# Kernel optimization log

Hardware: AMD Instinct MI355X
Metric: run time of the kernel (lower is better)

## Reference

```python
import jax, jax.numpy as jnp
import numpy as np

N = 6144
D_IN = 512
D_OUT = 512
DENSITY = 0.005


def setup_inputs() -> dict:
    key = jax.random.key(0)
    ks = jax.random.split(key, 12)
    x = jax.random.normal(ks[0], (N, D_IN), dtype=jnp.float32)
    adj_a = (jax.random.uniform(ks[1], (N, N)) < DENSITY).astype(jnp.float32)
    adj_b = (jax.random.uniform(ks[2], (N, N)) < DENSITY).astype(jnp.float32)
    # SparseAttention params (xavier-ish scale)
    W_sa = jax.random.normal(ks[3], (D_IN, D_OUT), dtype=jnp.float32) * (1.414 / np.sqrt(D_IN + D_OUT))
    a_sa = jax.random.normal(ks[4], (1, 2 * D_OUT), dtype=jnp.float32) * (1.414 / np.sqrt(1 + 2 * D_OUT))
    # GraphConvolution b params (uniform +-1/sqrt(out))
    stdv = 1.0 / np.sqrt(D_OUT)
    W_gcnb = jax.random.uniform(ks[5], (D_IN, D_OUT), minval=-stdv, maxval=stdv, dtype=jnp.float32)
    b_gcnb = jax.random.uniform(ks[6], (D_OUT,), minval=-stdv, maxval=stdv, dtype=jnp.float32)
    # gate Linear layers: Linear(2*D_IN, 1)
    s = 1.0 / np.sqrt(2 * D_IN)
    Wa = jax.random.uniform(ks[7], (1, 2 * D_IN), minval=-s, maxval=s, dtype=jnp.float32)
    ba = jax.random.uniform(ks[8], (1,), minval=-s, maxval=s, dtype=jnp.float32)
    Wb = jax.random.uniform(ks[9], (1, 2 * D_IN), minval=-s, maxval=s, dtype=jnp.float32)
    bb = jax.random.uniform(ks[10], (1,), minval=-s, maxval=s, dtype=jnp.float32)
    return {"x": x, "adj_a": adj_a, "adj_b": adj_b, "W_sa": W_sa, "a_sa": a_sa,
            "W_gcnb": W_gcnb, "b_gcnb": b_gcnb, "Wa": Wa, "ba": ba, "Wb": Wb, "bb": bb}


def reference(x, adj_a, adj_b, W_sa, a_sa, W_gcnb, b_gcnb, Wa, ba, Wb, bb):
    # type-level gates: sigmoid(Linear(cat[adj@x, x]))
    type_sum_a = adj_a @ x                      # [N, D_IN]
    type_sum_b = adj_b @ x
    attn_a = jax.nn.sigmoid(jnp.concatenate([type_sum_a, x], axis=1) @ Wa.T + ba)  # [N,1]
    attn_b = jax.nn.sigmoid(jnp.concatenate([type_sum_b, x], axis=1) @ Wb.T + bb)

    # SparseAttention over adj_a (edge pattern only)
    h = x @ W_sa                                # [N, D_OUT]
    Hd = h.shape[1]
    s_left = h @ a_sa[0, :Hd]                   # [N] contribution of source node i
    s_right = h @ a_sa[0, Hd:]                  # [N] contribution of target node j
    scores = s_left[:, None] + s_right[None, :]  # [N,N]
    e = jnp.where(adj_a != 0, jnp.exp(-jax.nn.leaky_relu(scores, 0.01)), 0.0)
    attn = e / (jnp.sum(e, axis=1, keepdims=True) + 1e-5)
    x_a = attn @ h                              # [N, D_OUT]

    # GCN branch over adj_b
    x_b = adj_b @ (x @ W_gcnb) + b_gcnb         # [N, D_OUT]

    return jax.nn.sigmoid(attn_a * x_a + attn_b * x_b)
```

## Files before the change

kernel.cpp:

```cpp
#include <hip/hip_runtime.h>
#include <math.h>

#define NN 6144
#define DD 512
#define CAP 128

typedef __bf16 bf16_t;
typedef __bf16 bf16x8 __attribute__((ext_vector_type(8)));
typedef unsigned short u16x8 __attribute__((ext_vector_type(8)));
typedef float f32x4 __attribute__((ext_vector_type(4)));

__device__ __forceinline__ float bf2f(unsigned short u) {
    unsigned v = ((unsigned)u) << 16;
    return __builtin_bit_cast(float, v);
}
__device__ __forceinline__ unsigned short f2bf(float f) {
    unsigned u = __builtin_bit_cast(unsigned, f);
    u += 0x7fffu + ((u >> 16) & 1u);
    return (unsigned short)(u >> 16);
}
__device__ __forceinline__ float sigmoidf_(float z) { return 1.0f / (1.0f + expf(-z)); }

__global__ __launch_bounds__(256) void k_prep(const float* __restrict__ Wsa,
                                              const float* __restrict__ Wg,
                                              const float* __restrict__ x,
                                              const float* __restrict__ Wa,
                                              const float* __restrict__ Wb,
                                              unsigned short* __restrict__ wt,
                                              float* __restrict__ xal, float* __restrict__ xar,
                                              float* __restrict__ xbl, float* __restrict__ xbr) {
    __shared__ float s[64][65];
    int bid = blockIdx.x;
    if (bid < 128) {
        int n0 = (bid & 15) * 64;
        int k0 = (bid >> 4) * 64;
        int tx = threadIdx.x & 63, ty = threadIdx.x >> 6;
        const float* src = (n0 < 512) ? Wsa : Wg;
        int nn0 = n0 & 511;
#pragma unroll
        for (int kk = 0; kk < 64; kk += 4)
            s[kk + ty][tx] = src[(size_t)(k0 + kk + ty) * 512 + nn0 + tx];
        __syncthreads();
#pragma unroll
        for (int nn = 0; nn < 64; nn += 4)
            wt[(size_t)(n0 + nn + ty) * 512 + k0 + tx] = f2bf(s[tx][nn + ty]);
    } else {
        int wave = threadIdx.x >> 6, lane = threadIdx.x & 63;
        int row = (bid - 128) * 4 + wave;
        int k0 = lane * 8;
        const float* xr_ = x + (size_t)row * DD + k0;
        float4 v0 = *(const float4*)xr_;
        float4 v1 = *(const float4*)(xr_ + 4);
        float xv[8] = {v0.x, v0.y, v0.z, v0.w, v1.x, v1.y, v1.z, v1.w};
        float a0 = 0, a1 = 0, b0 = 0, b1 = 0;
#pragma unroll
        for (int j = 0; j < 8; j++) {
            a0 += xv[j] * Wa[k0 + j];
            a1 += xv[j] * Wa[512 + k0 + j];
            b0 += xv[j] * Wb[k0 + j];
            b1 += xv[j] * Wb[512 + k0 + j];
        }
#pragma unroll
        for (int off = 32; off; off >>= 1) {
            a0 += __shfl_down(a0, off); a1 += __shfl_down(a1, off);
            b0 += __shfl_down(b0, off); b1 += __shfl_down(b1, off);
        }
        if (lane == 0) { xal[row] = a0; xar[row] = a1; xbl[row] = b0; xbr[row] = b1; }
    }
}

__global__ __launch_bounds__(256) void k_fused(const float* __restrict__ x,
                                               const bf16_t* __restrict__ wt,
                                               const float* __restrict__ adjA,
                                               const float* __restrict__ adjB,
                                               int* __restrict__ idxA, int* __restrict__ idxB,
                                               int* __restrict__ cntA, int* __restrict__ cntB,
                                               unsigned short* __restrict__ h,
                                               unsigned short* __restrict__ g) {
    int bid = blockIdx.x;
    int wave = threadIdx.x >> 6, lane = threadIdx.x & 63;
    int grp = bid % 5;
    if (grp < 4) {
        int sid = (bid / 5) * 4 + grp;
        int gw = sid * 4 + wave;
        int row = gw >> 1;
        int half = gw & 1;
        int which = row >= NN;
        int r = which ? row - NN : row;
        const float* adj = which ? adjB : adjA;
        int* idx = (which ? idxB : idxA) + (size_t)r * CAP;
        int* cnt = which ? cntB : cntA;

        const uint4* arow = (const uint4*)(adj + (size_t)r * NN) + half * 768 + lane;
        unsigned long long m = 0;
#pragma unroll
        for (int j = 0; j < 12; j++) {
            uint4 v = arow[j * 64];
            unsigned long long bits =
                (unsigned long long)(v.x != 0u) |
                ((unsigned long long)(v.y != 0u) << 1) |
                ((unsigned long long)(v.z != 0u) << 2) |
                ((unsigned long long)(v.w != 0u) << 3);
            m |= bits << (j * 4);
        }
        int c = (int)__popcll(m);
        int p = c;
#pragma unroll
        for (int off = 1; off < 64; off <<= 1) {
            int t = __shfl_up(p, off);
            if (lane >= off) p += t;
        }
        int total = __shfl(p, 63);
        int base = 0;
        if (lane == 0) base = atomicAdd(&cnt[r], total);
        base = __shfl(base, 0);
        int pos = base + p - c;
        while (m) {
            int b = __ffsll((long long)m) - 1;
            m &= m - 1;
            int col = ((half * 768) + ((b >> 2) * 64) + lane) * 4 + (b & 3);
            if (pos < CAP) idx[pos] = col;
            pos++;
        }
    } else {
        int tt = bid / 5;
        int row0 = (tt % (NN / 64)) * 64 + wave * 16;
        int col0 = (tt / (NN / 64)) * 64;
        int lr = lane & 15;
        int kg = (lane >> 4) * 8;

        f32x4 acc[4] = {{0,0,0,0},{0,0,0,0},{0,0,0,0},{0,0,0,0}};
        const float* ap = x + (size_t)(row0 + lr) * DD + kg;
        const bf16_t* bp = wt + (size_t)(col0 + lr) * DD + kg;

        for (int k0 = 0; k0 < DD; k0 += 32) {
            float4 a0 = *(const float4*)(ap + k0);
            float4 a1 = *(const float4*)(ap + k0 + 4);
            u16x8 au;
            au[0] = f2bf(a0.x); au[1] = f2bf(a0.y); au[2] = f2bf(a0.z); au[3] = f2bf(a0.w);
            au[4] = f2bf(a1.x); au[5] = f2bf(a1.y); au[6] = f2bf(a1.z); au[7] = f2bf(a1.w);
            bf16x8 a = __builtin_bit_cast(bf16x8, au);
#pragma unroll
            for (int n = 0; n < 4; n++) {
                bf16x8 b = *(const bf16x8*)(bp + (size_t)n * 16 * DD + k0);
                acc[n] = __builtin_amdgcn_mfma_f32_16x16x32_bf16(a, b, acc[n], 0, 0, 0);
            }
        }
        int dcol = lane & 15;
        int dr0 = (lane >> 4) * 4;
#pragma unroll
        for (int n = 0; n < 4; n++) {
            int col = col0 + n * 16 + dcol;
            unsigned short* dst = (col < 512) ? h : g;
            int cc = col & 511;
#pragma unroll
            for (int rr = 0; rr < 4; rr++) {
                int mr = row0 + dr0 + rr;
                dst[(size_t)mr * 512 + cc] = f2bf(acc[n][rr]);
            }
        }
    }
}

__global__ __launch_bounds__(256) void k_slr(const unsigned short* __restrict__ h,
                                             const float* __restrict__ a_sa,
                                             float* __restrict__ sl, float* __restrict__ sr) {
    int wave = threadIdx.x >> 6, lane = threadIdx.x & 63;
    int row = blockIdx.x * 4 + wave;
    int k0 = lane * 8;
    uint4 hv = *(const uint4*)(h + (size_t)row * DD + k0);
    unsigned u[4] = {hv.x, hv.y, hv.z, hv.w};
    float s0 = 0, s1 = 0;
#pragma unroll
    for (int j = 0; j < 4; j++) {
        float h0 = bf2f((unsigned short)(u[j] & 0xffff));
        float h1 = bf2f((unsigned short)(u[j] >> 16));
        s0 += h0 * a_sa[k0 + 2 * j] + h1 * a_sa[k0 + 2 * j + 1];
        s1 += h0 * a_sa[512 + k0 + 2 * j] + h1 * a_sa[512 + k0 + 2 * j + 1];
    }
#pragma unroll
    for (int off = 32; off; off >>= 1) { s0 += __shfl_down(s0, off); s1 += __shfl_down(s1, off); }
    if (lane == 0) { sl[row] = s0; sr[row] = s1; }
}

__global__ __launch_bounds__(256) void k_final(
    const int* __restrict__ idxA, const int* __restrict__ cntA,
    const int* __restrict__ idxB, const int* __restrict__ cntB,
    const unsigned short* __restrict__ h, const unsigned short* __restrict__ g,
    const float* __restrict__ sl, const float* __restrict__ sr,
    const float* __restrict__ xal, const float* __restrict__ xar,
    const float* __restrict__ xbl, const float* __restrict__ xbr,
    const float* __restrict__ ba, const float* __restrict__ bb,
    const float* __restrict__ bias, float* __restrict__ out) {
    int i = blockIdx.x;
    int tid = threadIdx.x;
    __shared__ float w[CAP];
    __shared__ int ja[CAP], jb[CAP];
    __shared__ float s_denom, s_ga, s_gb;

    int cA = cntA[i]; cA = cA > CAP ? CAP : cA;
    int cB = cntB[i]; cB = cB > CAP ? CAP : cB;
    if (tid < cA) {
        int j = idxA[(size_t)i * CAP + tid];
        ja[tid] = j;
        float s = sl[i] + sr[j];
        float lrelu = s > 0.f ? s : 0.01f * s;
        w[tid] = expf(-lrelu);
    }
    if (tid < cB) jb[tid] = idxB[(size_t)i * CAP + tid];
    __syncthreads();

    if (tid < 64) {
        float p = 0.f, gasum = 0.f, gbsum = 0.f;
        for (int t = tid; t < cA; t += 64) { p += w[t]; gasum += xal[ja[t]]; }
        for (int t = tid; t < cB; t += 64) gbsum += xbl[jb[t]];
#pragma unroll
        for (int off = 32; off; off >>= 1) {
            p += __shfl_down(p, off);
            gasum += __shfl_down(gasum, off);
            gbsum += __shfl_down(gbsum, off);
        }
        if (tid == 0) {
            s_denom = p;
            s_ga = sigmoidf_(gasum + xar[i] + ba[0]);
            s_gb = sigmoidf_(gbsum + xbr[i] + bb[0]);
        }
    }
    __syncthreads();
    float inv = 1.f / (s_denom + 1e-5f);
    float ga = s_ga, gb = s_gb;

    int d0 = tid * 2;
    float a0 = 0, a1 = 0, b0 = 0, b1 = 0;
#pragma unroll 4
    for (int t = 0; t < cA; t++) {
        unsigned hv = *(const unsigned*)(h + (size_t)ja[t] * 512 + d0);
        float wt_ = w[t];
        a0 += wt_ * bf2f((unsigned short)(hv & 0xffff));
        a1 += wt_ * bf2f((unsigned short)(hv >> 16));
    }
#pragma unroll 4
    for (int t = 0; t < cB; t++) {
        unsigned gv = *(const unsigned*)(g + (size_t)jb[t] * 512 + d0);
        b0 += bf2f((unsigned short)(gv & 0xffff));
        b1 += bf2f((unsigned short)(gv >> 16));
    }
    float z0 = ga * (a0 * inv) + gb * (b0 + bias[d0]);
    float z1 = ga * (a1 * inv) + gb * (b1 + bias[d0 + 1]);
    out[(size_t)i * 512 + d0]     = sigmoidf_(z0);
    out[(size_t)i * 512 + d0 + 1] = sigmoidf_(z1);
}

extern "C" void kernel_launch(void* const* d_in, const int* in_sizes, int n_in,
                              void* d_out, int out_size, void* d_ws, size_t ws_size,
                              hipStream_t stream) {
    const float* x    = (const float*)d_in[0];
    const float* adjA = (const float*)d_in[1];
    const float* adjB = (const float*)d_in[2];
    const float* Wsa  = (const float*)d_in[3];
    const float* a_sa = (const float*)d_in[4];
    const float* Wg   = (const float*)d_in[5];
    const float* bg   = (const float*)d_in[6];
    const float* Wa   = (const float*)d_in[7];
    const float* ba   = (const float*)d_in[8];
    const float* Wb   = (const float*)d_in[9];
    const float* bb   = (const float*)d_in[10];
    float* out = (float*)d_out;

    char* ws = (char*)d_ws;
    size_t off = 0;
    auto alloc = [&](size_t bytes) -> void* {
        void* p = ws + off;
        off += (bytes + 255) & ~(size_t)255;
        return p;
    };
    unsigned short* wt = (unsigned short*)alloc((size_t)1024 * DD * 2);
    unsigned short* h  = (unsigned short*)alloc((size_t)NN * DD * 2);
    unsigned short* g  = (unsigned short*)alloc((size_t)NN * DD * 2);
    int* idxA = (int*)alloc((size_t)NN * CAP * 4);
    int* idxB = (int*)alloc((size_t)NN * CAP * 4);
    int* cntA = (int*)alloc((size_t)NN * 4 * 2);
    int* cntB = cntA + NN;
    float* xal = (float*)alloc((size_t)NN * 4);
    float* xar = (float*)alloc((size_t)NN * 4);
    float* xbl = (float*)alloc((size_t)NN * 4);
    float* xbr = (float*)alloc((size_t)NN * 4);
    float* sl = (float*)alloc((size_t)NN * 4);
    float* sr = (float*)alloc((size_t)NN * 4);

    hipMemsetAsync(cntA, 0, (size_t)NN * 4 * 2, stream);
    k_prep<<<128 + NN / 4, 256, 0, stream>>>(Wsa, Wg, x, Wa, Wb, wt, xal, xar, xbl, xbr);
    k_fused<<<7680, 256, 0, stream>>>(x, (const bf16_t*)wt, adjA, adjB,
                                      idxA, idxB, cntA, cntB, h, g);
    k_slr<<<NN / 4, 256, 0, stream>>>(h, a_sa, sl, sr);
    k_final<<<NN, 256, 0, stream>>>(idxA, cntA, idxB, cntB, h, g, sl, sr,
                                    xal, xar, xbl, xbr, ba, bb, bg, out);
}
```

Baseline: 180.7 us.

## Store adjacency bitmasks and compact them in final kernel; fold s_left/right into x projection

The adjacency scan now writes raw 64-bit nonzero masks per lane instead of compacting indices with atomics, and the final kernel does the prefix-scan compaction into shared memory. This removes the memset, the atomics and the global index arrays. The attention score vectors are computed as x·(W_sa·a) in the same pass as the gate projections, which drops the separate k_slr kernel and one launch. The trade-off is that s_left/s_right now use fp32 x rather than bf16 h, and the final kernel does extra scan work per row.

```diff
diff --git a/kernel.cpp b/kernel.cpp
--- a/kernel.cpp
+++ b/kernel.cpp
@@ -9,6 +9,7 @@
 typedef __bf16 bf16x8 __attribute__((ext_vector_type(8)));
 typedef unsigned short u16x8 __attribute__((ext_vector_type(8)));
 typedef float f32x4 __attribute__((ext_vector_type(4)));
+typedef unsigned u32x4 __attribute__((ext_vector_type(4)));
 
 __device__ __forceinline__ float bf2f(unsigned short u) {
     unsigned v = ((unsigned)u) << 16;
@@ -23,14 +24,12 @@
 
 __global__ __launch_bounds__(256) void k_prep(const float* __restrict__ Wsa,
                                               const float* __restrict__ Wg,
-                                              const float* __restrict__ x,
-                                              const float* __restrict__ Wa,
-                                              const float* __restrict__ Wb,
+                                              const float* __restrict__ a_sa,
                                               unsigned short* __restrict__ wt,
-                                              float* __restrict__ xal, float* __restrict__ xar,
-                                              float* __restrict__ xbl, float* __restrict__ xbr) {
+                                              float* __restrict__ wsl, float* __restrict__ wsr) {
     __shared__ float s[64][65];
     int bid = blockIdx.x;
+    int wave = threadIdx.x >> 6, lane = threadIdx.x & 63;
     if (bid < 128) {
         int n0 = (bid & 15) * 64;
         int k0 = (bid >> 4) * 64;
@@ -45,147 +44,133 @@
         for (int nn = 0; nn < 64; nn += 4)
             wt[(size_t)(n0 + nn + ty) * 512 + k0 + tx] = f2bf(s[tx][nn + ty]);
     } else {
-        int wave = threadIdx.x >> 6, lane = threadIdx.x & 63;
-        int row = (bid - 128) * 4 + wave;
+        int k = (bid - 128) * 4 + wave;
+        int n0 = lane * 8;
+        const float* wr = Wsa + (size_t)k * 512 + n0;
+        float4 w0 = *(const float4*)wr, w1 = *(const float4*)(wr + 4);
+        float4 l0 = *(const float4*)(a_sa + n0), l1 = *(const float4*)(a_sa + n0 + 4);
+        float4 r0 = *(const float4*)(a_sa + 512 + n0), r1 = *(const float4*)(a_sa + 512 + n0 + 4);
+        float sl_ = w0.x*l0.x + w0.y*l0.y + w0.z*l0.z + w0.w*l0.w
+                  + w1.x*l1.x + w1.y*l1.y + w1.z*l1.z + w1.w*l1.w;
+        float sr_ = w0.x*r0.x + w0.y*r0.y + w0.z*r0.z + w0.w*r0.w
+                  + w1.x*r1.x + w1.y*r1.y + w1.z*r1.z + w1.w*r1.w;
+#pragma unroll
+        for (int off = 32; off; off >>= 1) { sl_ += __shfl_down(sl_, off); sr_ += __shfl_down(sr_, off); }
+        if (lane == 0) { wsl[k] = sl_; wsr[k] = sr_; }
+    }
+}
+
+__global__ __launch_bounds__(256) void k_fused(const float* __restrict__ x,
+                                               const bf16_t* __restrict__ wt,
+                                               const float* __restrict__ adjA,
+                                               const float* __restrict__ adjB,
+                                               const float* __restrict__ Wa,
+                                               const float* __restrict__ Wb,
+                                               const float* __restrict__ wsl,
+                                               const float* __restrict__ wsr,
+                                               unsigned long long* __restrict__ maskbuf,
+                                               unsigned short* __restrict__ h,
+                                               unsigned short* __restrict__ g,
+                                               float* __restrict__ xal, float* __restrict__ xar,
+                                               float* __restrict__ xbl, float* __restrict__ xbr,
+                                               float* __restrict__ sl, float* __restrict__ sr) {
+    int bid = blockIdx.x;
+    int wave = threadIdx.x >> 6, lane = threadIdx.x & 63;
+    if (bid < 7680) {
+        int grp = bid % 5;
+        if (grp < 4) {
+            int sid = (bid / 5) * 4 + grp;
+            int gw = sid * 4 + wave;
+            int row = gw >> 1;
+            int half = gw & 1;
+            int which = row >= NN;
+            int r = which ? row - NN : row;
+            const float* adj = which ? adjB : adjA;
+            const u32x4* arow = (const u32x4*)(adj + (size_t)r * NN) + half * 768 + lane;
+            u32x4 v[12];
+#pragma unroll
+            for (int j = 0; j < 12; j++) v[j] = arow[j * 64];
+            unsigned long long m = 0;
+#pragma unroll
+            for (int j = 0; j < 12; j++) {
+                unsigned long long bits =
+                    (unsigned long long)(v[j][0] != 0u) |
+                    ((unsigned long long)(v[j][1] != 0u) << 1) |
+                    ((unsigned long long)(v[j][2] != 0u) << 2) |
+                    ((unsigned long long)(v[j][3] != 0u) << 3);
+                m |= bits << (j * 4);
+            }
+            maskbuf[(size_t)gw * 64 + lane] = m;
+        } else {
+            int tt = bid / 5;
+            int row0 = (tt % (NN / 64)) * 64 + wave * 16;
+            int col0 = (tt / (NN / 64)) * 64;
+            int lr = lane & 15;
+            int kg = (lane >> 4) * 8;
+
+            f32x4 acc[4] = {{0,0,0,0},{0,0,0,0},{0,0,0,0},{0,0,0,0}};
+            const float* ap = x + (size_t)(row0 + lr) * DD + kg;
+            const bf16_t* bp = wt + (size_t)(col0 + lr) * DD + kg;
+
+            for (int k0 = 0; k0 < DD; k0 += 32) {
+                float4 a0 = *(const float4*)(ap + k0);
+                float4 a1 = *(const float4*)(ap + k0 + 4);
+                u16x8 au;
+                au[0] = f2bf(a0.x); au[1] = f2bf(a0.y); au[2] = f2bf(a0.z); au[3] = f2bf(a0.w);
+                au[4] = f2bf(a1.x); au[5] = f2bf(a1.y); au[6] = f2bf(a1.z); au[7] = f2bf(a1.w);
+                bf16x8 a = __builtin_bit_cast(bf16x8, au);
+#pragma unroll
+                for (int n = 0; n < 4; n++) {
+                    bf16x8 b = *(const bf16x8*)(bp + (size_t)n * 16 * DD + k0);
+                    acc[n] = __builtin_amdgcn_mfma_f32_16x16x32_bf16(a, b, acc[n], 0, 0, 0);
+                }
+            }
+            int dcol = lane & 15;
+            int dr0 = (lane >> 4) * 4;
+#pragma unroll
+            for (int n = 0; n < 4; n++) {
+                int col = col0 + n * 16 + dcol;
+                unsigned short* dst = (col < 512) ? h : g;
+                int cc = col & 511;
+#pragma unroll
+                for (int rr = 0; rr < 4; rr++) {
+                    int mr = row0 + dr0 + rr;
+                    dst[(size_t)mr * 512 + cc] = f2bf(acc[n][rr]);
+                }
+            }
+        }
+    } else {
+        int pid = bid - 7680;
+        int row = pid * 4 + wave;
         int k0 = lane * 8;
         const float* xr_ = x + (size_t)row * DD + k0;
         float4 v0 = *(const float4*)xr_;
         float4 v1 = *(const float4*)(xr_ + 4);
         float xv[8] = {v0.x, v0.y, v0.z, v0.w, v1.x, v1.y, v1.z, v1.w};
-        float a0 = 0, a1 = 0, b0 = 0, b1 = 0;
-#pragma unroll
-        for (int j = 0; j < 8; j++) {
-            a0 += xv[j] * Wa[k0 + j];
-            a1 += xv[j] * Wa[512 + k0 + j];
-            b0 += xv[j] * Wb[k0 + j];
-            b1 += xv[j] * Wb[512 + k0 + j];
-        }
-#pragma unroll
-        for (int off = 32; off; off >>= 1) {
-            a0 += __shfl_down(a0, off); a1 += __shfl_down(a1, off);
-            b0 += __shfl_down(b0, off); b1 += __shfl_down(b1, off);
-        }
-        if (lane == 0) { xal[row] = a0; xar[row] = a1; xbl[row] = b0; xbr[row] = b1; }
-    }
-}
-
-__global__ __launch_bounds__(256) void k_fused(const float* __restrict__ x,
-                                               const bf16_t* __restrict__ wt,
-                                               const float* __restrict__ adjA,
-                                               const float* __restrict__ adjB,
-                                               int* __restrict__ idxA, int* __restrict__ idxB,
-                                               int* __restrict__ cntA, int* __restrict__ cntB,
-                                               unsigned short* __restrict__ h,
-                                               unsigned short* __restrict__ g) {
-    int bid = blockIdx.x;
-    int wave = threadIdx.x >> 6, lane = threadIdx.x & 63;
-    int grp = bid % 5;
-    if (grp < 4) {
-        int sid = (bid / 5) * 4 + grp;
-        int gw = sid * 4 + wave;
-        int row = gw >> 1;
-        int half = gw & 1;
-        int which = row >= NN;
-        int r = which ? row - NN : row;
-        const float* adj = which ? adjB : adjA;
-        int* idx = (which ? idxB : idxA) + (size_t)r * CAP;
-        int* cnt = which ? cntB : cntA;
-
-        const uint4* arow = (const uint4*)(adj + (size_t)r * NN) + half * 768 + lane;
-        unsigned long long m = 0;
-#pragma unroll
-        for (int j = 0; j < 12; j++) {
-            uint4 v = arow[j * 64];
-            unsigned long long bits =
-                (unsigned long long)(v.x != 0u) |
-                ((unsigned long long)(v.y != 0u) << 1) |
-                ((unsigned long long)(v.z != 0u) << 2) |
-                ((unsigned long long)(v.w != 0u) << 3);
-            m |= bits << (j * 4);
-        }
-        int c = (int)__popcll(m);
-        int p = c;
-#pragma unroll
-        for (int off = 1; off < 64; off <<= 1) {
-            int t = __shfl_up(p, off);
-            if (lane >= off) p += t;
-        }
-        int total = __shfl(p, 63);
-        int base = 0;
-        if (lane == 0) base = atomicAdd(&cnt[r], total);
-        base = __shfl(base, 0);
-        int pos = base + p - c;
-        while (m) {
-            int b = __ffsll((long long)m) - 1;
-            m &= m - 1;
-            int col = ((half * 768) + ((b >> 2) * 64) + lane) * 4 + (b & 3);
-            if (pos < CAP) idx[pos] = col;
-            pos++;
-        }
-    } else {
-        int tt = bid / 5;
-        int row0 = (tt % (NN / 64)) * 64 + wave * 16;
-        int col0 = (tt / (NN / 64)) * 64;
-        int lr = lane & 15;
-        int kg = (lane >> 4) * 8;
-
-        f32x4 acc[4] = {{0,0,0,0},{0,0,0,0},{0,0,0,0},{0,0,0,0}};
-        const float* ap = x + (size_t)(row0 + lr) * DD + kg;
-        const bf16_t* bp = wt + (size_t)(col0 + lr) * DD + kg;
-
-        for (int k0 = 0; k0 < DD; k0 += 32) {
-            float4 a0 = *(const float4*)(ap + k0);
-            float4 a1 = *(const float4*)(ap + k0 + 4);
-            u16x8 au;
-            au[0] = f2bf(a0.x); au[1] = f2bf(a0.y); au[2] = f2bf(a0.z); au[3] = f2bf(a0.w);
-            au[4] = f2bf(a1.x); au[5] = f2bf(a1.y); au[6] = f2bf(a1.z); au[7] = f2bf(a1.w);
-            bf16x8 a = __builtin_bit_cast(bf16x8, au);
-#pragma unroll
-            for (int n = 0; n < 4; n++) {
-                bf16x8 b = *(const bf16x8*)(bp + (size_t)n * 16 * DD + k0);
-                acc[n] = __builtin_amdgcn_mfma_f32_16x16x32_bf16(a, b, acc[n], 0, 0, 0);
-            }
-        }
-        int dcol = lane & 15;
-        int dr0 = (lane >> 4) * 4;
-#pragma unroll
-        for (int n = 0; n < 4; n++) {
-            int col = col0 + n * 16 + dcol;
-            unsigned short* dst = (col < 512) ? h : g;
-            int cc = col & 511;
-#pragma unroll
-            for (int rr = 0; rr < 4; rr++) {
-                int mr = row0 + dr0 + rr;
-                dst[(size_t)mr * 512 + cc] = f2bf(acc[n][rr]);
-            }
-        }
-    }
-}
-
-__global__ __launch_bounds__(256) void k_slr(const unsigned short* __restrict__ h,
-                                             const float* __restrict__ a_sa,
-                                             float* __restrict__ sl, float* __restrict__ sr) {
-    int wave = threadIdx.x >> 6, lane = threadIdx.x & 63;
-    int row = blockIdx.x * 4 + wave;
-    int k0 = lane * 8;
-    uint4 hv = *(const uint4*)(h + (size_t)row * DD + k0);
-    unsigned u[4] = {hv.x, hv.y, hv.z, hv.w};
-    float s0 = 0, s1 = 0;
-#pragma unroll
-    for (int j = 0; j < 4; j++) {
-        float h0 = bf2f((unsigned short)(u[j] & 0xffff));
-        float h1 = bf2f((unsigned short)(u[j] >> 16));
-        s0 += h0 * a_sa[k0 + 2 * j] + h1 * a_sa[k0 + 2 * j + 1];
-        s1 += h0 * a_sa[512 + k0 + 2 * j] + h1 * a_sa[512 + k0 + 2 * j + 1];
-    }
-#pragma unroll
-    for (int off = 32; off; off >>= 1) { s0 += __shfl_down(s0, off); s1 += __shfl_down(s1, off); }
-    if (lane == 0) { sl[row] = s0; sr[row] = s1; }
+        float d[6] = {0, 0, 0, 0, 0, 0};
+        const float* srcs[6] = {Wa + k0, Wa + 512 + k0, Wb + k0, Wb + 512 + k0, wsl + k0, wsr + k0};
+#pragma unroll
+        for (int q = 0; q < 6; q++) {
+            float4 w0 = *(const float4*)srcs[q];
+            float4 w1 = *(const float4*)(srcs[q] + 4);
+            float wv[8] = {w0.x, w0.y, w0.z, w0.w, w1.x, w1.y, w1.z, w1.w};
+#pragma unroll
+            for (int j = 0; j < 8; j++) d[q] += xv[j] * wv[j];
+        }
+#pragma unroll
+        for (int off = 32; off; off >>= 1)
+#pragma unroll
+            for (int q = 0; q < 6; q++) d[q] += __shfl_down(d[q], off);
+        if (lane == 0) {
+            xal[row] = d[0]; xar[row] = d[1];
+            xbl[row] = d[2]; xbr[row] = d[3];
+            sl[row] = d[4]; sr[row] = d[5];
+        }
+    }
 }
 
 __global__ __launch_bounds__(256) void k_final(
-    const int* __restrict__ idxA, const int* __restrict__ cntA,
-    const int* __restrict__ idxB, const int* __restrict__ cntB,
+    const unsigned long long* __restrict__ maskbuf,
     const unsigned short* __restrict__ h, const unsigned short* __restrict__ g,
     const float* __restrict__ sl, const float* __restrict__ sr,
     const float* __restrict__ xal, const float* __restrict__ xar,
@@ -194,34 +179,58 @@
     const float* __restrict__ bias, float* __restrict__ out) {
     int i = blockIdx.x;
     int tid = threadIdx.x;
+    int wave = tid >> 6, lane = tid & 63;
     __shared__ float w[CAP];
     __shared__ int ja[CAP], jb[CAP];
+    __shared__ int tot[4];
     __shared__ float s_denom, s_ga, s_gb;
 
-    int cA = cntA[i]; cA = cA > CAP ? CAP : cA;
-    int cB = cntB[i]; cB = cB > CAP ? CAP : cB;
+    int half = wave & 1;
+    int gw = (wave < 2) ? (i * 2 + half) : ((NN + i) * 2 + half);
+    unsigned long long m = maskbuf[(size_t)gw * 64 + lane];
+    int c = __popcll(m);
+    int p = c;
+#pragma unroll
+    for (int off = 1; off < 64; off <<= 1) {
+        int t = __shfl_up(p, off);
+        if (lane >= off) p += t;
+    }
+    if (lane == 63) tot[wave] = p;
+    __syncthreads();
+    int base = (wave == 1) ? tot[0] : (wave == 3) ? tot[2] : 0;
+    int pos = base + p - c;
+    int* dst = (wave < 2) ? ja : jb;
+    while (m) {
+        int b = __ffsll((long long)m) - 1;
+        m &= m - 1;
+        int col = half * 3072 + (((b >> 2) * 64 + lane) << 2) + (b & 3);
+        if (pos < CAP) dst[pos] = col;
+        pos++;
+    }
+    __syncthreads();
+    int cA = tot[0] + tot[1]; cA = cA > CAP ? CAP : cA;
+    int cB = tot[2] + tot[3]; cB = cB > CAP ? CAP : cB;
+
     if (tid < cA) {
-        int j = idxA[(size_t)i * CAP + tid];
-        ja[tid] = j;
+        int j = ja[tid];
         float s = sl[i] + sr[j];
         float lrelu = s > 0.f ? s : 0.01f * s;
         w[tid] = expf(-lrelu);
     }
-    if (tid < cB) jb[tid] = idxB[(size_t)i * CAP + tid];
     __syncthreads();
 
     if (tid < 64) {
-        float p = 0.f, gasum = 0.f, gbsum = 0.f;
-        for (int t = tid; t < cA; t += 64) { p += w[t]; gasum += xal[ja[t]]; }
+        float p2 = 0.f, gasum = 0.f, gbsum = 0.f;
+        for (int t = tid; t < cA; t += 64) { p2 += w[t]; gasum += xal[ja[t]]; }
         for (int t = tid; t < cB; t += 64) gbsum += xbl[jb[t]];
 #pragma unroll
         for (int off = 32; off; off >>= 1) {
-            p += __shfl_down(p, off);
+            p2 += __shfl_down(p2, off);
             gasum += __shfl_down(gasum, off);
             gbsum += __shfl_down(gbsum, off);
         }
         if (tid == 0) {
-            s_denom = p;
+            s_denom = p2;
             s_ga = sigmoidf_(gasum + xar[i] + ba[0]);
             s_gb = sigmoidf_(gbsum + xbr[i] + bb[0]);
         }
@@ -277,22 +286,19 @@
     unsigned short* wt = (unsigned short*)alloc((size_t)1024 * DD * 2);
     unsigned short* h  = (unsigned short*)alloc((size_t)NN * DD * 2);
     unsigned short* g  = (unsigned short*)alloc((size_t)NN * DD * 2);
-    int* idxA = (int*)alloc((size_t)NN * CAP * 4);
-    int* idxB = (int*)alloc((size_t)NN * CAP * 4);
-    int* cntA = (int*)alloc((size_t)NN * 4 * 2);
-    int* cntB = cntA + NN;
+    unsigned long long* maskbuf = (unsigned long long*)alloc((size_t)24576 * 64 * 8);
     float* xal = (float*)alloc((size_t)NN * 4);
     float* xar = (float*)alloc((size_t)NN * 4);
     float* xbl = (float*)alloc((size_t)NN * 4);
     float* xbr = (float*)alloc((size_t)NN * 4);
-    float* sl = (float*)alloc((size_t)NN * 4);
-    float* sr = (float*)alloc((size_t)NN * 4);
-
-    hipMemsetAsync(cntA, 0, (size_t)NN * 4 * 2, stream);
-    k_prep<<<128 + NN / 4, 256, 0, stream>>>(Wsa, Wg, x, Wa, Wb, wt, xal, xar, xbl, xbr);
-    k_fused<<<7680, 256, 0, stream>>>(x, (const bf16_t*)wt, adjA, adjB,
-                                      idxA, idxB, cntA, cntB, h, g);
-    k_slr<<<NN / 4, 256, 0, stream>>>(h, a_sa, sl, sr);
-    k_final<<<NN, 256, 0, stream>>>(idxA, cntA, idxB, cntB, h, g, sl, sr,
-                                    xal, xar, xbl, xbr, ba, bb, bg, out);
-}
+    float* sl  = (float*)alloc((size_t)NN * 4);
+    float* sr  = (float*)alloc((size_t)NN * 4);
+    float* wsl = (float*)alloc((size_t)DD * 4);
+    float* wsr = (float*)alloc((size_t)DD * 4);
+
+    k_prep<<<256, 256, 0, stream>>>(Wsa, Wg, a_sa, wt, wsl, wsr);
+    k_fused<<<9216, 256, 0, stream>>>(x, (const bf16_t*)wt, adjA, adjB, Wa, Wb, wsl, wsr,
+                                      maskbuf, h, g, xal, xar, xbl, xbr, sl, sr);
+    k_final<<<NN, 256, 0, stream>>>(maskbuf, h, g, sl, sr, xal, xar, xbl, xbr,
+                                    ba, bb, bg, out);
+}
```

After: 172.3 us. 1.05x faster.
